# Optimization experiments

Measured on AMD Instinct MI355X. Metric: run time of the kernel, lower is better.

Reference implementation:

```python
import jax, jax.numpy as jnp
import numpy as np

B, S, D, H, E, K = 2, 2048, 1024, 2048, 8, 2


def setup_inputs() -> dict:
    key = jax.random.key(0)
    ks = jax.random.split(key, 9)
    sc_d = 1.0 / np.sqrt(D)
    sc_h = 1.0 / np.sqrt(H)
    return {
        "x": jax.random.normal(ks[0], (B, S, D), dtype=jnp.float32),
        "w_router": jax.random.normal(ks[1], (E, D), dtype=jnp.float32) * sc_d,
        "Wg": jax.random.normal(ks[2], (E, H, D), dtype=jnp.float32) * sc_d,  # per-expert gate proj (torch Linear weight layout [out,in])
        "Wu": jax.random.normal(ks[3], (E, H, D), dtype=jnp.float32) * sc_d,
        "Wd": jax.random.normal(ks[4], (E, D, H), dtype=jnp.float32) * sc_h,
        "sg": jax.random.normal(ks[5], (H, D), dtype=jnp.float32) * sc_d,  # shared expert
        "su": jax.random.normal(ks[6], (H, D), dtype=jnp.float32) * sc_d,
        "sd": jax.random.normal(ks[7], (D, H), dtype=jnp.float32) * sc_h,
    }


def reference(x, w_router, Wg, Wu, Wd, sg, su, sd):
    b, s, d = x.shape
    xf = x.reshape(-1, d)  # [T, D]

    # --- gating ---
    logits = jnp.einsum("td,ed->te", xf, w_router)
    probs = jax.nn.softmax(logits, axis=-1)  # [T, E]
    topw, topi = jax.lax.top_k(probs, K)  # [T, K]
    topw = topw / jnp.sum(topw, axis=-1, keepdims=True)
    # combine weights per (token, expert): topk indices are distinct per token
    comb = jnp.sum(topw[..., None] * jax.nn.one_hot(topi, E, dtype=xf.dtype), axis=1)  # [T, E]

    # --- shared expert (SwiGLU) ---
    shared = jnp.einsum(
        "th,dh->td",
        jax.nn.silu(jnp.einsum("td,hd->th", xf, sg)) * jnp.einsum("td,hd->th", xf, su),
        sd,
    )

    # --- routed experts: dense all-expert compute, weighted combine ---
    h1 = jax.nn.silu(jnp.einsum("td,ehd->teh", xf, Wg))
    h2 = jnp.einsum("td,ehd->teh", xf, Wu)
    eo = jnp.einsum("teh,edh->ted", h1 * h2, Wd)  # [T, E, D]
    routed = jnp.einsum("te,ted->td", comb, eo)

    return (routed + shared).reshape(b, s, d)
```

## Files before the change

### kernel.cpp

```cpp
#include <hip/hip_runtime.h>
#include <hip/hip_bf16.h>

#define T_TOK 4096
#define D_DIM 1024
#define H_DIM 2048

typedef __attribute__((ext_vector_type(8))) short short8;
typedef __attribute__((ext_vector_type(4))) float floatx4;

__device__ __forceinline__ unsigned short f2bf(float f) {
  unsigned int u = __builtin_bit_cast(unsigned int, f);
  return (unsigned short)((u + 0x7fffu + ((u >> 16) & 1u)) >> 16);
}

__device__ __forceinline__ float bf2f(unsigned short s) {
  unsigned int u = ((unsigned int)s) << 16;
  return __builtin_bit_cast(float, u);
}

__device__ __forceinline__ void glds16(const ushort* g, ushort* l) {
  __builtin_amdgcn_global_load_lds(
      (const __attribute__((address_space(1))) unsigned int*)g,
      (__attribute__((address_space(3))) unsigned int*)l, 16, 0, 0);
}

__global__ void prep_kernel(const float4* __restrict__ Wg, ushort4* __restrict__ Wgb,
                            const float4* __restrict__ Wu, ushort4* __restrict__ Wub,
                            const float4* __restrict__ Wd, ushort4* __restrict__ Wdb,
                            const float4* __restrict__ sg, ushort4* __restrict__ sgb,
                            const float4* __restrict__ su, ushort4* __restrict__ sub,
                            const float4* __restrict__ sd, ushort4* __restrict__ sdb,
                            const float* __restrict__ x, const float* __restrict__ wr,
                            ushort* __restrict__ xb,
                            int* __restrict__ topi, float2* __restrict__ topw) {
  if (blockIdx.x < 55296) {
    int id = blockIdx.x * 256 + threadIdx.x;
    const float4* s; ushort4* d; int i;
    if (id < 4194304)       { s = Wg; d = Wgb; i = id; }
    else if (id < 8388608)  { s = Wu; d = Wub; i = id - 4194304; }
    else if (id < 12582912) { s = Wd; d = Wdb; i = id - 8388608; }
    else if (id < 13107200) { s = sg; d = sgb; i = id - 12582912; }
    else if (id < 13631488) { s = su; d = sub; i = id - 13107200; }
    else                    { s = sd; d = sdb; i = id - 13631488; }
    float4 v = s[i];
    ushort4 o;
    o.x = f2bf(v.x); o.y = f2bf(v.y); o.z = f2bf(v.z); o.w = f2bf(v.w);
    d[i] = o;
    return;
  }
  const int w = threadIdx.x >> 6;
  const int l = threadIdx.x & 63;
  const int t = (blockIdx.x - 55296) * 4 + w;
  const float4* xr = (const float4*)(x + (size_t)t * D_DIM);
  ushort4* xo = (ushort4*)(xb + (size_t)t * D_DIM);
  float p[8];
#pragma unroll
  for (int e = 0; e < 8; ++e) p[e] = 0.f;
#pragma unroll
  for (int i = 0; i < 4; ++i) {
    float4 xv = xr[i * 64 + l];
    ushort4 o;
    o.x = f2bf(xv.x); o.y = f2bf(xv.y); o.z = f2bf(xv.z); o.w = f2bf(xv.w);
    xo[i * 64 + l] = o;
#pragma unroll
    for (int e = 0; e < 8; ++e) {
      float4 wv = ((const float4*)(wr + e * D_DIM))[i * 64 + l];
      p[e] += xv.x * wv.x + xv.y * wv.y + xv.z * wv.z + xv.w * wv.w;
    }
  }
#pragma unroll
  for (int off = 32; off > 0; off >>= 1) {
#pragma unroll
    for (int e = 0; e < 8; ++e) p[e] += __shfl_xor(p[e], off, 64);
  }
  if (l == 0) {
    float mx = p[0];
#pragma unroll
    for (int e = 1; e < 8; ++e) mx = fmaxf(mx, p[e]);
    float pr[8];
#pragma unroll
    for (int e = 0; e < 8; ++e) pr[e] = __expf(p[e] - mx);
    int i0 = 0;
#pragma unroll
    for (int e = 1; e < 8; ++e) if (pr[e] > pr[i0]) i0 = e;
    int i1 = (i0 == 0) ? 1 : 0;
#pragma unroll
    for (int e = 0; e < 8; ++e) if (e != i0 && pr[e] > pr[i1]) i1 = e;
    float w0 = pr[i0], w1 = pr[i1];
    float inv = 1.f / (w0 + w1);
    topi[t] = i0 | (i1 << 8);
    topw[t] = make_float2(w0 * inv, w1 * inv);
  }
}

__global__ void build_lists_kernel(const int* __restrict__ topi,
                                   int* __restrict__ counts, int* __restrict__ list,
                                   int* __restrict__ pos) {
  const int e = blockIdx.x;
  const int tid = threadIdx.x;
  const int l = tid & 63;
  const int w = tid >> 6;
  __shared__ int wtot[4];
  int base = 0;
  for (int c = 0; c < T_TOK; c += 256) {
    int t = c + tid;
    int ti = topi[t];
    int e0 = ti & 255, e1 = ti >> 8;
    bool flag = (e0 == e) || (e1 == e);
    unsigned long long m = __ballot(flag);
    int lanepos = __popcll(m & ((1ull << l) - 1ull));
    if (l == 0) wtot[w] = __popcll(m);
    __syncthreads();
    int waveoff = 0;
#pragma unroll
    for (int i = 0; i < 4; ++i) waveoff += (i < w) ? wtot[i] : 0;
    int tot = wtot[0] + wtot[1] + wtot[2] + wtot[3];
    if (flag) {
      int p = base + waveoff + lanepos;
      list[e * T_TOK + p] = t;
      int slot = (e0 == e) ? 0 : 1;
      pos[t * 2 + slot] = p;
    }
    base += tot;
    __syncthreads();
  }
  if (tid == 0) counts[e] = base;
}

__global__ __launch_bounds__(256, 2)
void gemm1_kernel(const ushort* __restrict__ xb,
                  const ushort* __restrict__ Wgb, const ushort* __restrict__ Wub,
                  const ushort* __restrict__ sgb, const ushort* __restrict__ sub,
                  const int* __restrict__ list, const int* __restrict__ counts,
                  ushort* __restrict__ h) {
  const int e = blockIdx.z;
  int n_e, hbase;
  {
    int acc = 0, ce = 0;
    for (int q = 0; q < 8; ++q) {
      int c = counts[q];
      if (q < e) acc += c;
      if (q == e) ce = c;
    }
    n_e = (e == 8) ? T_TOK : ce;
    hbase = (e == 8) ? 8192 : acc;
  }
  const int r0 = blockIdx.y * 128;
  if (r0 >= n_e) return;
  const int c0 = blockIdx.x * 128;
  const ushort* Wg = (e == 8) ? sgb : (Wgb + (size_t)e * H_DIM * D_DIM);
  const ushort* Wu = (e == 8) ? sub : (Wub + (size_t)e * H_DIM * D_DIM);
  const int hrow0 = hbase + r0;

  __shared__ __align__(16) ushort As[128 * 64];
  __shared__ __align__(16) ushort Bgs[128 * 64];
  __shared__ __align__(16) ushort Bus[128 * 64];
  __shared__ int toks[128];

  const int tid = threadIdx.x;
  const int l = tid & 63;
  const int w = tid >> 6;

  if (tid < 128) {
    int rr = r0 + tid;
    toks[tid] = (e == 8) ? ((rr < T_TOK) ? rr : (T_TOK - 1))
                         : list[e * T_TOK + ((rr < n_e) ? rr : (n_e - 1))];
  }
  __syncthreads();

  const int lrow8 = l >> 3;
  const int csw = (((l & 7) ^ lrow8) << 3);
  const ushort* ap[4];
#pragma unroll
  for (int i = 0; i < 4; ++i) {
    int ri = (w * 4 + i) * 8 + lrow8;
    ap[i] = xb + (size_t)toks[ri] * D_DIM + csw;
  }
  const ushort* bgp = Wg + (size_t)(c0 + w * 32 + lrow8) * D_DIM + csw;
  const ushort* bup = Wu + (size_t)(c0 + w * 32 + lrow8) * D_DIM + csw;

  floatx4 accg[4][4], accu[4][4];
#pragma unroll
  for (int i = 0; i < 4; ++i)
#pragma unroll
    for (int j = 0; j < 4; ++j) {
      accg[i][j] = (floatx4)(0.f);
      accu[i][j] = (floatx4)(0.f);
    }

  const int mrow = (w & 1) * 64;
  const int ncol = (w >> 1) * 64;
  int rba[4], rbb[4];
#pragma unroll
  for (int i = 0; i < 4; ++i) {
    rba[i] = (mrow + 16 * i + (l & 15)) * 64;
    rbb[i] = (ncol + 16 * i + (l & 15)) * 64;
  }

  for (int k0 = 0; k0 < D_DIM; k0 += 64) {
    __syncthreads();
#pragma unroll
    for (int i = 0; i < 4; ++i) {
      glds16(ap[i] + k0,                As  + (w * 4 + i) * 512);
      glds16(bgp + k0 + i * 8 * D_DIM,  Bgs + (w * 4 + i) * 512);
      glds16(bup + k0 + i * 8 * D_DIM,  Bus + (w * 4 + i) * 512);
    }
    __syncthreads();
#pragma unroll
    for (int s = 0; s < 2; ++s) {
      const int pq = ((((s << 2) | (l >> 4)) ^ (l & 7)) << 3);
      short8 a[4], bg[4], bu[4];
#pragma unroll
      for (int i = 0; i < 4; ++i) a[i] = *(const short8*)(As + rba[i] + pq);
#pragma unroll
      for (int j = 0; j < 4; ++j) {
        bg[j] = *(const short8*)(Bgs + rbb[j] + pq);
        bu[j] = *(const short8*)(Bus + rbb[j] + pq);
      }
#pragma unroll
      for (int i = 0; i < 4; ++i)
#pragma unroll
        for (int j = 0; j < 4; ++j) {
          accg[i][j] = __builtin_amdgcn_mfma_f32_16x16x32_bf16(a[i], bg[j], accg[i][j], 0, 0, 0);
          accu[i][j] = __builtin_amdgcn_mfma_f32_16x16x32_bf16(a[i], bu[j], accu[i][j], 0, 0, 0);
        }
    }
  }

#pragma unroll
  for (int i = 0; i < 4; ++i) {
#pragma unroll
    for (int r = 0; r < 4; ++r) {
      int lrow = mrow + 16 * i + (l >> 4) * 4 + r;
      if (r0 + lrow < n_e) {
#pragma unroll
        for (int j = 0; j < 4; ++j) {
          float g = accg[i][j][r];
          float u = accu[i][j][r];
          float hv = (g / (1.f + __expf(-g))) * u;
          int col = c0 + ncol + 16 * j + (l & 15);
          h[(size_t)(hrow0 + lrow) * H_DIM + col] = f2bf(hv);
        }
      }
    }
  }
}

__global__ __launch_bounds__(256, 2)
void gemm2_kernel(const ushort* __restrict__ h,
                  const ushort* __restrict__ Wdb, const ushort* __restrict__ sdb,
                  const int* __restrict__ counts,
                  ushort* __restrict__ eo) {
  const int e = blockIdx.z;
  int n_e, hbase;
  {
    int acc = 0, ce = 0;
    for (int q = 0; q < 8; ++q) {
      int c = counts[q];
      if (q < e) acc += c;
      if (q == e) ce = c;
    }
    n_e = (e == 8) ? T_TOK : ce;
    hbase = (e == 8) ? 8192 : acc;
  }
  const int r0 = blockIdx.y * 128;
  if (r0 >= n_e) return;
  const int c0 = blockIdx.x * 256;
  const ushort* Wd = (e == 8) ? sdb : (Wdb + (size_t)e * D_DIM * H_DIM);
  const int hrow0 = hbase + r0;

  __shared__ __align__(16) ushort As[128 * 64];
  __shared__ __align__(16) ushort Bs[256 * 64];

  const int tid = threadIdx.x;
  const int l = tid & 63;
  const int w = tid >> 6;

  const int lrow8 = l >> 3;
  const int csw = (((l & 7) ^ lrow8) << 3);
  const ushort* apb = h  + (size_t)(hrow0 + w * 32 + lrow8) * H_DIM + csw;
  const ushort* bpb = Wd + (size_t)(c0 + w * 64 + lrow8) * H_DIM + csw;

  floatx4 acc[4][8];
#pragma unroll
  for (int i = 0; i < 4; ++i)
#pragma unroll
    for (int j = 0; j < 8; ++j) acc[i][j] = (floatx4)(0.f);

  const int mrow = (w & 1) * 64;
  const int ncol = (w >> 1) * 128;
  int rba[4], rbb[8];
#pragma unroll
  for (int i = 0; i < 4; ++i) rba[i] = (mrow + 16 * i + (l & 15)) * 64;
#pragma unroll
  for (int j = 0; j < 8; ++j) rbb[j] = (ncol + 16 * j + (l & 15)) * 64;

  for (int k0 = 0; k0 < H_DIM; k0 += 64) {
    __syncthreads();
#pragma unroll
    for (int i = 0; i < 4; ++i)
      glds16(apb + k0 + i * 8 * H_DIM, As + (w * 4 + i) * 512);
#pragma unroll
    for (int i = 0; i < 8; ++i)
      glds16(bpb + k0 + i * 8 * H_DIM, Bs + (w * 8 + i) * 512);
    __syncthreads();
#pragma unroll
    for (int s = 0; s < 2; ++s) {
      const int pq = ((((s << 2) | (l >> 4)) ^ (l & 7)) << 3);
      short8 a[4], b[8];
#pragma unroll
      for (int i = 0; i < 4; ++i) a[i] = *(const short8*)(As + rba[i] + pq);
#pragma unroll
      for (int j = 0; j < 8; ++j) b[j] = *(const short8*)(Bs + rbb[j] + pq);
#pragma unroll
      for (int i = 0; i < 4; ++i)
#pragma unroll
        for (int j = 0; j < 8; ++j)
          acc[i][j] = __builtin_amdgcn_mfma_f32_16x16x32_bf16(a[i], b[j], acc[i][j], 0, 0, 0);
    }
  }

#pragma unroll
  for (int i = 0; i < 4; ++i) {
#pragma unroll
    for (int r = 0; r < 4; ++r) {
      int lrow = mrow + 16 * i + (l >> 4) * 4 + r;
      if (r0 + lrow < n_e) {
#pragma unroll
        for (int j = 0; j < 8; ++j) {
          int col = c0 + ncol + 16 * j + (l & 15);
          eo[(size_t)(hrow0 + lrow) * D_DIM + col] = f2bf(acc[i][j][r]);
        }
      }
    }
  }
}

__global__ void combine_kernel(const ushort* __restrict__ eo, const int* __restrict__ topi,
                               const float2* __restrict__ topw, const int* __restrict__ pos,
                               const int* __restrict__ counts, float* __restrict__ out) {
  const int t = blockIdx.x;
  const int c4 = threadIdx.x;
  int ti = topi[t];
  int e0 = ti & 255, e1 = ti >> 8;
  int off0 = 0, off1 = 0;
#pragma unroll
  for (int q = 0; q < 8; ++q) {
    int c = counts[q];
    off0 += (q < e0) ? c : 0;
    off1 += (q < e1) ? c : 0;
  }
  float2 wv = topw[t];
  int2 p = ((const int2*)pos)[t];
  const ushort4* ra = (const ushort4*)(eo + (size_t)(off0 + p.x) * D_DIM);
  const ushort4* rb = (const ushort4*)(eo + (size_t)(off1 + p.y) * D_DIM);
  const ushort4* rs = (const ushort4*)(eo + (size_t)(8192 + t) * D_DIM);
  ushort4 a = ra[c4], b = rb[c4], s = rs[c4];
  float4 o;
  o.x = wv.x * bf2f(a.x) + wv.y * bf2f(b.x) + bf2f(s.x);
  o.y = wv.x * bf2f(a.y) + wv.y * bf2f(b.y) + bf2f(s.y);
  o.z = wv.x * bf2f(a.z) + wv.y * bf2f(b.z) + bf2f(s.z);
  o.w = wv.x * bf2f(a.w) + wv.y * bf2f(b.w) + bf2f(s.w);
  ((float4*)(out + (size_t)t * D_DIM))[c4] = o;
}

#define OFF_XB   0ull
#define OFF_WGB  (OFF_XB + 8388608ull)
#define OFF_WUB  (OFF_WGB + 33554432ull)
#define OFF_WDB  (OFF_WUB + 33554432ull)
#define OFF_SGB  (OFF_WDB + 33554432ull)
#define OFF_SUB  (OFF_SGB + 4194304ull)
#define OFF_SDB  (OFF_SUB + 4194304ull)
#define OFF_H    (OFF_SDB + 4194304ull)
#define OFF_EO   OFF_WGB
#define OFF_CNT  (OFF_H + 50331648ull)
#define OFF_LIST (OFF_CNT + 64ull)
#define OFF_POS  (OFF_LIST + 131072ull)
#define OFF_TOPI (OFF_POS + 32768ull)
#define OFF_TOPW (OFF_TOPI + 16384ull)

extern "C" void kernel_launch(void* const* d_in, const int* in_sizes, int n_in,
                              void* d_out, int out_size, void* d_ws, size_t ws_size,
                              hipStream_t stream) {
  const float* x  = (const float*)d_in[0];
  const float* wr = (const float*)d_in[1];
  const float* Wg = (const float*)d_in[2];
  const float* Wu = (const float*)d_in[3];
  const float* Wd = (const float*)d_in[4];
  const float* sg = (const float*)d_in[5];
  const float* su = (const float*)d_in[6];
  const float* sd = (const float*)d_in[7];
  float* out = (float*)d_out;
  char* ws = (char*)d_ws;

  ushort* xb  = (ushort*)(ws + OFF_XB);
  ushort* Wgb = (ushort*)(ws + OFF_WGB);
  ushort* Wub = (ushort*)(ws + OFF_WUB);
  ushort* Wdb = (ushort*)(ws + OFF_WDB);
  ushort* sgb = (ushort*)(ws + OFF_SGB);
  ushort* sub = (ushort*)(ws + OFF_SUB);
  ushort* sdb = (ushort*)(ws + OFF_SDB);
  ushort* hbuf = (ushort*)(ws + OFF_H);
  ushort* eo   = (ushort*)(ws + OFF_EO);
  int* counts = (int*)(ws + OFF_CNT);
  int* list   = (int*)(ws + OFF_LIST);
  int* pos    = (int*)(ws + OFF_POS);
  int* topi   = (int*)(ws + OFF_TOPI);
  float2* topw = (float2*)(ws + OFF_TOPW);

  prep_kernel<<<56320, 256, 0, stream>>>((const float4*)Wg, (ushort4*)Wgb,
                                         (const float4*)Wu, (ushort4*)Wub,
                                         (const float4*)Wd, (ushort4*)Wdb,
                                         (const float4*)sg, (ushort4*)sgb,
                                         (const float4*)su, (ushort4*)sub,
                                         (const float4*)sd, (ushort4*)sdb,
                                         x, wr, xb, topi, topw);
  build_lists_kernel<<<8, 256, 0, stream>>>(topi, counts, list, pos);

  gemm1_kernel<<<dim3(16, 32, 9), 256, 0, stream>>>(xb, Wgb, Wub, sgb, sub,
                                                    list, counts, hbuf);
  gemm2_kernel<<<dim3(4, 32, 9), 256, 0, stream>>>(hbuf, Wdb, sdb, counts, eo);
  combine_kernel<<<4096, 256, 0, stream>>>(eo, topi, topw, pos, counts, out);
}
```

Before: 441.0 us.

## Restructure gate/up GEMM into 256x256 double-buffered pipelined tiles with 8 waves

The gate/up GEMM kernel moves to 512 threads with 256-row token tiles. The gate and up weight rows are interleaved into one 256-wide B tile, so a single accumulator array holds both projections. Global-to-LDS loads are double-buffered in 32-wide k halves and interleaved with MFMA phases, using explicit barriers, waitcnt, sched_barrier and setprio. The goal is to hide load latency and raise arithmetic intensity per LDS byte, at the cost of more register pressure and more padded work for small expert counts.

```diff
diff --git a/kernel.cpp b/kernel.cpp
--- a/kernel.cpp
+++ b/kernel.cpp
@@ -127,7 +127,7 @@
   if (tid == 0) counts[e] = base;
 }
 
-__global__ __launch_bounds__(256, 2)
+__global__ __launch_bounds__(512, 2)
 void gemm1_kernel(const ushort* __restrict__ xb,
                   const ushort* __restrict__ Wgb, const ushort* __restrict__ Wub,
                   const ushort* __restrict__ sgb, const ushort* __restrict__ sub,
@@ -136,109 +136,177 @@
   const int e = blockIdx.z;
   int n_e, hbase;
   {
-    int acc = 0, ce = 0;
+    int acc0 = 0, ce = 0;
     for (int q = 0; q < 8; ++q) {
       int c = counts[q];
-      if (q < e) acc += c;
+      if (q < e) acc0 += c;
       if (q == e) ce = c;
     }
     n_e = (e == 8) ? T_TOK : ce;
-    hbase = (e == 8) ? 8192 : acc;
-  }
-  const int r0 = blockIdx.y * 128;
+    hbase = (e == 8) ? 8192 : acc0;
+  }
+  const int r0 = blockIdx.y * 256;
   if (r0 >= n_e) return;
   const int c0 = blockIdx.x * 128;
   const ushort* Wg = (e == 8) ? sgb : (Wgb + (size_t)e * H_DIM * D_DIM);
   const ushort* Wu = (e == 8) ? sub : (Wub + (size_t)e * H_DIM * D_DIM);
   const int hrow0 = hbase + r0;
 
-  __shared__ __align__(16) ushort As[128 * 64];
-  __shared__ __align__(16) ushort Bgs[128 * 64];
-  __shared__ __align__(16) ushort Bus[128 * 64];
-  __shared__ int toks[128];
+  __shared__ __align__(16) ushort Ab[2][2][256 * 32];
+  __shared__ __align__(16) ushort Bb[2][2][256 * 32];
+  __shared__ int toks[256];
 
   const int tid = threadIdx.x;
   const int l = tid & 63;
   const int w = tid >> 6;
 
-  if (tid < 128) {
+  if (tid < 256) {
     int rr = r0 + tid;
     toks[tid] = (e == 8) ? ((rr < T_TOK) ? rr : (T_TOK - 1))
                          : list[e * T_TOK + ((rr < n_e) ? rr : (n_e - 1))];
   }
   __syncthreads();
 
-  const int lrow8 = l >> 3;
-  const int csw = (((l & 7) ^ lrow8) << 3);
-  const ushort* ap[4];
-#pragma unroll
-  for (int i = 0; i < 4; ++i) {
-    int ri = (w * 4 + i) * 8 + lrow8;
-    ap[i] = xb + (size_t)toks[ri] * D_DIM + csw;
-  }
-  const ushort* bgp = Wg + (size_t)(c0 + w * 32 + lrow8) * D_DIM + csw;
-  const ushort* bup = Wu + (size_t)(c0 + w * 32 + lrow8) * D_DIM + csw;
-
-  floatx4 accg[4][4], accu[4][4];
-#pragma unroll
-  for (int i = 0; i < 4; ++i)
-#pragma unroll
-    for (int j = 0; j < 4; ++j) {
-      accg[i][j] = (floatx4)(0.f);
-      accu[i][j] = (floatx4)(0.f);
-    }
-
-  const int mrow = (w & 1) * 64;
-  const int ncol = (w >> 1) * 64;
-  int rba[4], rbb[4];
-#pragma unroll
-  for (int i = 0; i < 4; ++i) {
-    rba[i] = (mrow + 16 * i + (l & 15)) * 64;
-    rbb[i] = (ncol + 16 * i + (l & 15)) * 64;
-  }
-
-  for (int k0 = 0; k0 < D_DIM; k0 += 64) {
-    __syncthreads();
-#pragma unroll
-    for (int i = 0; i < 4; ++i) {
-      glds16(ap[i] + k0,                As  + (w * 4 + i) * 512);
-      glds16(bgp + k0 + i * 8 * D_DIM,  Bgs + (w * 4 + i) * 512);
-      glds16(bup + k0 + i * 8 * D_DIM,  Bus + (w * 4 + i) * 512);
-    }
-    __syncthreads();
-#pragma unroll
-    for (int s = 0; s < 2; ++s) {
-      const int pq = ((((s << 2) | (l >> 4)) ^ (l & 7)) << 3);
-      short8 a[4], bg[4], bu[4];
-#pragma unroll
-      for (int i = 0; i < 4; ++i) a[i] = *(const short8*)(As + rba[i] + pq);
-#pragma unroll
-      for (int j = 0; j < 4; ++j) {
-        bg[j] = *(const short8*)(Bgs + rbb[j] + pq);
-        bu[j] = *(const short8*)(Bus + rbb[j] + pq);
-      }
-#pragma unroll
-      for (int i = 0; i < 4; ++i)
-#pragma unroll
-        for (int j = 0; j < 4; ++j) {
-          accg[i][j] = __builtin_amdgcn_mfma_f32_16x16x32_bf16(a[i], bg[j], accg[i][j], 0, 0, 0);
-          accu[i][j] = __builtin_amdgcn_mfma_f32_16x16x32_bf16(a[i], bu[j], accu[i][j], 0, 0, 0);
-        }
-    }
-  }
-
-#pragma unroll
-  for (int i = 0; i < 4; ++i) {
+  const int lchunk = (((l & 3) ^ ((l >> 3) & 3)) << 3);
+  const ushort* asrc[2];
+  const ushort* bsrc[2];
+#pragma unroll
+  for (int c = 0; c < 2; ++c) {
+    int r = 32 * w + 16 * c + (l >> 2);
+    asrc[c] = xb + (size_t)toks[r] * D_DIM + lchunk;
+    int f = r >> 4, j = r & 15;
+    const ushort* Wm = (f & 1) ? Wu : Wg;
+    int hcol = c0 + 32 * (f >> 2) + 16 * ((f >> 1) & 1) + j;
+    bsrc[c] = Wm + (size_t)hcol * D_DIM + lchunk;
+  }
+
+  const int wm = w >> 2, wn = w & 3;
+  const int rl = l & 15;
+  const int pch = (((l >> 4) ^ ((rl >> 1) & 3)) << 3);
+  int aoff[8], boff[4];
+#pragma unroll
+  for (int i = 0; i < 8; ++i) aoff[i] = (128 * wm + 16 * i + rl) * 32 + pch;
+#pragma unroll
+  for (int j = 0; j < 4; ++j) boff[j] = (64 * wn + 16 * j + rl) * 32 + pch;
+
+  floatx4 acc[8][4];
+#pragma unroll
+  for (int i = 0; i < 8; ++i)
+#pragma unroll
+    for (int j = 0; j < 4; ++j) acc[i][j] = (floatx4)(0.f);
+
+#pragma unroll
+  for (int c = 0; c < 2; ++c) glds16(asrc[c],      &Ab[0][0][(32 * w + 16 * c) * 32]);
+#pragma unroll
+  for (int c = 0; c < 2; ++c) glds16(bsrc[c],      &Bb[0][0][(32 * w + 16 * c) * 32]);
+#pragma unroll
+  for (int c = 0; c < 2; ++c) glds16(asrc[c] + 32, &Ab[0][1][(32 * w + 16 * c) * 32]);
+#pragma unroll
+  for (int c = 0; c < 2; ++c) glds16(bsrc[c] + 32, &Bb[0][1][(32 * w + 16 * c) * 32]);
+  asm volatile("s_waitcnt vmcnt(4)" ::: "memory");
+  __builtin_amdgcn_s_barrier();
+
+  for (int t = 0; t < 16; ++t) {
+    const int d = t & 1, dn = d ^ 1;
+    const int kn = (t + 1) * 64;
+    const bool st = (t < 15);
+    short8 a[4], b[4];
+
+#pragma unroll
+    for (int i = 0; i < 4; ++i) a[i] = *(const short8*)(&Ab[d][0][aoff[i]]);
+#pragma unroll
+    for (int j = 0; j < 4; ++j) b[j] = *(const short8*)(&Bb[d][0][boff[j]]);
+    if (st) {
+#pragma unroll
+      for (int c = 0; c < 2; ++c) glds16(asrc[c] + kn, &Ab[dn][0][(32 * w + 16 * c) * 32]);
+    }
+    __builtin_amdgcn_s_barrier();
+    asm volatile("s_waitcnt lgkmcnt(0)" ::: "memory");
+    __builtin_amdgcn_sched_barrier(0);
+    __builtin_amdgcn_s_setprio(1);
+#pragma unroll
+    for (int i = 0; i < 4; ++i)
+#pragma unroll
+      for (int j = 0; j < 4; ++j)
+        acc[i][j] = __builtin_amdgcn_mfma_f32_16x16x32_bf16(a[i], b[j], acc[i][j], 0, 0, 0);
+    __builtin_amdgcn_s_setprio(0);
+    __builtin_amdgcn_sched_barrier(0);
+    __builtin_amdgcn_s_barrier();
+
+#pragma unroll
+    for (int i = 0; i < 4; ++i) a[i] = *(const short8*)(&Ab[d][0][aoff[4 + i]]);
+    if (st) {
+#pragma unroll
+      for (int c = 0; c < 2; ++c) glds16(bsrc[c] + kn, &Bb[dn][0][(32 * w + 16 * c) * 32]);
+    }
+    __builtin_amdgcn_s_barrier();
+    asm volatile("s_waitcnt lgkmcnt(0)" ::: "memory");
+    __builtin_amdgcn_sched_barrier(0);
+    __builtin_amdgcn_s_setprio(1);
+#pragma unroll
+    for (int i = 0; i < 4; ++i)
+#pragma unroll
+      for (int j = 0; j < 4; ++j)
+        acc[4 + i][j] = __builtin_amdgcn_mfma_f32_16x16x32_bf16(a[i], b[j], acc[4 + i][j], 0, 0, 0);
+    __builtin_amdgcn_s_setprio(0);
+    __builtin_amdgcn_sched_barrier(0);
+    asm volatile("s_waitcnt vmcnt(4)" ::: "memory");
+    __builtin_amdgcn_s_barrier();
+
+#pragma unroll
+    for (int i = 0; i < 4; ++i) a[i] = *(const short8*)(&Ab[d][1][aoff[i]]);
+#pragma unroll
+    for (int j = 0; j < 4; ++j) b[j] = *(const short8*)(&Bb[d][1][boff[j]]);
+    if (st) {
+#pragma unroll
+      for (int c = 0; c < 2; ++c) glds16(asrc[c] + kn + 32, &Ab[dn][1][(32 * w + 16 * c) * 32]);
+    }
+    __builtin_amdgcn_s_barrier();
+    asm volatile("s_waitcnt lgkmcnt(0)" ::: "memory");
+    __builtin_amdgcn_sched_barrier(0);
+    __builtin_amdgcn_s_setprio(1);
+#pragma unroll
+    for (int i = 0; i < 4; ++i)
+#pragma unroll
+      for (int j = 0; j < 4; ++j)
+        acc[i][j] = __builtin_amdgcn_mfma_f32_16x16x32_bf16(a[i], b[j], acc[i][j], 0, 0, 0);
+    __builtin_amdgcn_s_setprio(0);
+    __builtin_amdgcn_sched_barrier(0);
+    __builtin_amdgcn_s_barrier();
+
+#pragma unroll
+    for (int i = 0; i < 4; ++i) a[i] = *(const short8*)(&Ab[d][1][aoff[4 + i]]);
+    if (st) {
+#pragma unroll
+      for (int c = 0; c < 2; ++c) glds16(bsrc[c] + kn + 32, &Bb[dn][1][(32 * w + 16 * c) * 32]);
+    }
+    __builtin_amdgcn_s_barrier();
+    asm volatile("s_waitcnt lgkmcnt(0)" ::: "memory");
+    __builtin_amdgcn_sched_barrier(0);
+    __builtin_amdgcn_s_setprio(1);
+#pragma unroll
+    for (int i = 0; i < 4; ++i)
+#pragma unroll
+      for (int j = 0; j < 4; ++j)
+        acc[4 + i][j] = __builtin_amdgcn_mfma_f32_16x16x32_bf16(a[i], b[j], acc[4 + i][j], 0, 0, 0);
+    __builtin_amdgcn_s_setprio(0);
+    __builtin_amdgcn_sched_barrier(0);
+    asm volatile("s_waitcnt vmcnt(4)" ::: "memory");
+    __builtin_amdgcn_s_barrier();
+  }
+
+#pragma unroll
+  for (int m = 0; m < 8; ++m) {
 #pragma unroll
     for (int r = 0; r < 4; ++r) {
-      int lrow = mrow + 16 * i + (l >> 4) * 4 + r;
+      int lrow = 128 * wm + 16 * m + (l >> 4) * 4 + r;
       if (r0 + lrow < n_e) {
 #pragma unroll
-        for (int j = 0; j < 4; ++j) {
-          float g = accg[i][j][r];
-          float u = accu[i][j][r];
+        for (int j2 = 0; j2 < 2; ++j2) {
+          float g = acc[m][2 * j2][r];
+          float u = acc[m][2 * j2 + 1][r];
           float hv = (g / (1.f + __expf(-g))) * u;
-          int col = c0 + ncol + 16 * j + (l & 15);
+          int col = c0 + 32 * wn + 16 * j2 + rl;
           h[(size_t)(hrow0 + lrow) * H_DIM + col] = f2bf(hv);
         }
       }
@@ -417,7 +485,7 @@
                                          x, wr, xb, topi, topw);
   build_lists_kernel<<<8, 256, 0, stream>>>(topi, counts, list, pos);
 
-  gemm1_kernel<<<dim3(16, 32, 9), 256, 0, stream>>>(xb, Wgb, Wub, sgb, sub,
+  gemm1_kernel<<<dim3(16, 16, 9), 512, 0, stream>>>(xb, Wgb, Wub, sgb, sub,
                                                     list, counts, hbuf);
   gemm2_kernel<<<dim3(4, 32, 9), 256, 0, stream>>>(hbuf, Wdb, sdb, counts, eo);
   combine_kernel<<<4096, 256, 0, stream>>>(eo, topi, topw, pos, counts, out);
```

New measurement: 480.8 us. +9.0%, slower.
